# Performance work log

Measured on AMD Instinct MI355X. Metric: run time of the kernel, lower is better.

The kernel has to match this reference:

```python
import math
import jax, jax.numpy as jnp
import numpy as np

NUM_HEADS = 16
WINDOW = 64  # neighbor_size
NEG_INF = -1e30


def setup_inputs() -> dict:
    key = jax.random.key(0)
    ks = jax.random.split(key, 5)
    B, L, D = 2, 2048, 1024
    x = jax.random.normal(ks[0], (B, L, D), dtype=jnp.float32)
    s = 0.02
    Wq = jax.random.normal(ks[1], (D, D), dtype=jnp.float32) * s
    Wk = jax.random.normal(ks[2], (D, D), dtype=jnp.float32) * s
    Wv = jax.random.normal(ks[3], (D, D), dtype=jnp.float32) * s
    Wo = jax.random.normal(ks[4], (D, D), dtype=jnp.float32) * s
    return {
        "x": x, "Wq": Wq, "Wk": Wk, "Wv": Wv, "Wo": Wo,
        "sep_gate": jnp.float32(0.1),
        "align_gate": jnp.float32(0.1),
        "coh_gate": jnp.float32(0.1),
    }


def reference(x, Wq, Wk, Wv, Wo, sep_gate, align_gate, coh_gate):
    B, L, D = x.shape
    H = NUM_HEADS
    hd = D // H
    scale = math.sqrt(hd)

    # projections (torch Linear: y = x @ W.T), split heads -> (B, H, L, hd)
    def proj(W):
        return (x @ W.T).reshape(B, L, H, hd).transpose(0, 2, 1, 3)

    q, k, v = proj(Wq), proj(Wk), proj(Wv)

    # raw scores (B, H, L, L)
    scores = jnp.einsum("bhqd,bhkd->bhqk", q, k) / scale

    # Reynolds rules (applied BEFORE masking, mean over full kv dim, as in source)
    similarity = jax.nn.sigmoid(scores)
    separation = -sep_gate * similarity ** 2
    alignment = align_gate * scores
    score_mean = jnp.mean(scores, axis=-1, keepdims=True)
    cohesion = -coh_gate * jnp.abs(scores - score_mean)
    scores = scores + separation + alignment + cohesion

    # causal sliding-window mask: attend iff 0 <= i - j < WINDOW
    i = jnp.arange(L)[:, None]
    j = jnp.arange(L)[None, :]
    dist = i - j
    masked = (dist < 0) | (dist >= WINDOW)  # (L, L) True = blocked
    scores = jnp.where(masked[None, None, :, :], NEG_INF, scores)

    attn = jax.nn.softmax(scores, axis=-1)  # dropout p=0.0 -> identity
    out = jnp.einsum("bhqk,bhkd->bhqd", attn, v)
    out = out.transpose(0, 2, 1, 3).reshape(B, L, D)
    return out @ Wo.T
```

## Files before the change

kernel.cpp:

```cpp
#include <hip/hip_runtime.h>
#include <math.h>

#define L_SEQ 2048
#define DMODEL 1024
#define HEADS 16
#define HD 64
#define BATCH 2
#define MROWS (BATCH*L_SEQ)
#define KDIM 1024
#define VSTRIDE 2136

typedef short bfrag8 __attribute__((ext_vector_type(8)));
typedef float f32x4f __attribute__((ext_vector_type(4)));

__device__ __forceinline__ unsigned short f2bf(float f) {
    unsigned u = __float_as_uint(f);
    unsigned r = u + 0x7FFFu + ((u >> 16) & 1u);
    return (unsigned short)(r >> 16);
}
__device__ __forceinline__ float bf2f(unsigned short h) {
    return __uint_as_float(((unsigned)h) << 16);
}

__global__ __launch_bounds__(256) void convert_bf16(
    const float* __restrict__ x, const float* __restrict__ wq,
    const float* __restrict__ wk, const float* __restrict__ wv,
    const float* __restrict__ wo,
    unsigned short* __restrict__ xb, unsigned short* __restrict__ qwb,
    unsigned short* __restrict__ kwb, unsigned short* __restrict__ vwb,
    unsigned short* __restrict__ owb, float* __restrict__ kmean_acc)
{
    const int bid = blockIdx.x;
    if (bid == 8192) {
        float4 z = make_float4(0.f, 0.f, 0.f, 0.f);
        *(float4*)&kmean_acc[threadIdx.x * 8]     = z;
        *(float4*)&kmean_acc[threadIdx.x * 8 + 4] = z;
        return;
    }
    const float* src; unsigned short* dst; size_t base;
    if (bid < 4096) { src = x; dst = xb; base = (size_t)bid * 1024; }
    else {
        const int r = bid - 4096; const int w = r >> 10; const int off = r & 1023;
        src = (w==0) ? wq : (w==1) ? wk : (w==2) ? wv : wo;
        dst = (w==0) ? qwb : (w==1) ? kwb : (w==2) ? vwb : owb;
        base = (size_t)off * 1024;
    }
    const size_t idx = base + (size_t)threadIdx.x * 4;
    float4 v = *(const float4*)&src[idx];
    ushort4 o;
    o.x = f2bf(v.x); o.y = f2bf(v.y); o.z = f2bf(v.z); o.w = f2bf(v.w);
    *(ushort4*)&dst[idx] = o;
}

#define GBK 64

__global__ void mfma_gemm_qkv(
    const unsigned short* __restrict__ A,
    const unsigned short* __restrict__ W0, const unsigned short* __restrict__ W1,
    const unsigned short* __restrict__ W2,
    unsigned short* __restrict__ qo, unsigned short* __restrict__ ko,
    unsigned short* __restrict__ vo, float* __restrict__ kmean_acc)
{
    __shared__ short As[128*GBK];
    __shared__ short Bs[128*GBK];

    const int tid  = threadIdx.x;
    const int wave = tid >> 6, lane = tid & 63;
    const int m0   = blockIdx.x * 128;
    const int n0g  = blockIdx.y * 128;

    const int which = n0g >> 10;
    const int n0 = n0g & 1023;
    const unsigned short* Wp = (which==0) ? W0 : (which==1) ? W1 : W2;

    const int quad = lane >> 4, lm = lane & 15;
    const int wm = wave >> 1, wn = wave & 1;

    f32x4f acc[4][4] = {};

    const int se   = wave * 2048 + lane * 8;
    const int srow = se >> 6;
    const int scg  = (se & 63) >> 3;
    const int sgcol = ((scg ^ (srow & 7)) << 3);

    for (int k0 = 0; k0 < KDIM; k0 += GBK) {
        __syncthreads();
        #pragma unroll
        for (int i = 0; i < 4; ++i) {
            const int ebase = wave * 2048 + i * 512;
            const int row = srow + i * 8;
            __builtin_amdgcn_global_load_lds(
                (const __attribute__((address_space(1))) void*)(A + (size_t)(m0 + row) * KDIM + k0 + sgcol),
                (__attribute__((address_space(3))) void*)(&As[ebase]), 16, 0, 0);
            __builtin_amdgcn_global_load_lds(
                (const __attribute__((address_space(1))) void*)(Wp + (size_t)(n0 + row) * KDIM + k0 + sgcol),
                (__attribute__((address_space(3))) void*)(&Bs[ebase]), 16, 0, 0);
        }
        __syncthreads();

        #pragma unroll
        for (int kk = 0; kk < 2; ++kk) {
            bfrag8 af[4], bf[4];
            #pragma unroll
            for (int t = 0; t < 4; ++t) {
                const int ar = wm*64 + t*16 + lm;
                af[t] = *(const bfrag8*)&As[ar*GBK + (((kk*4 + quad) ^ (ar & 7)) << 3)];
                const int br = wn*64 + t*16 + lm;
                bf[t] = *(const bfrag8*)&Bs[br*GBK + (((kk*4 + quad) ^ (br & 7)) << 3)];
            }
            #pragma unroll
            for (int mt = 0; mt < 4; ++mt)
                #pragma unroll
                for (int nt = 0; nt < 4; ++nt)
                    acc[mt][nt] = __builtin_amdgcn_mfma_f32_16x16x32_bf16(
                        af[mt], bf[nt], acc[mt][nt], 0, 0, 0);
        }
    }

    if (which == 2) {
        #pragma unroll
        for (int mt = 0; mt < 4; ++mt)
            #pragma unroll
            for (int nt = 0; nt < 4; ++nt) {
                const int gn = n0 + wn*64 + nt*16 + lm;
                const int h = gn >> 6, d = gn & 63;
                const int gm0 = m0 + wm*64 + mt*16 + quad*4;
                const int b = gm0 >> 11, l0 = gm0 & (L_SEQ-1);
                ushort4 o;
                o.x = f2bf(acc[mt][nt][0]); o.y = f2bf(acc[mt][nt][1]);
                o.z = f2bf(acc[mt][nt][2]); o.w = f2bf(acc[mt][nt][3]);
                *(ushort4*)&vo[((size_t)((b*HEADS + h)*HD + d))*VSTRIDE + 64 + l0] = o;
            }
    } else {
        unsigned short* Cp = (which==0) ? qo : ko;
        #pragma unroll
        for (int mt = 0; mt < 4; ++mt)
            #pragma unroll
            for (int nt = 0; nt < 4; ++nt) {
                const int gn = n0 + wn*64 + nt*16 + lm;
                const int h = gn >> 6, d = gn & 63;
                #pragma unroll
                for (int r = 0; r < 4; ++r) {
                    const int gm = m0 + wm*64 + mt*16 + quad*4 + r;
                    const int b = gm >> 11, l = gm & (L_SEQ-1);
                    Cp[(((size_t)(b*HEADS + h) * L_SEQ) + l) * HD + d] = f2bf(acc[mt][nt][r]);
                }
            }
        if (which == 1) {
            const int b = m0 >> 11;
            #pragma unroll
            for (int nt = 0; nt < 4; ++nt) {
                const int gn = n0 + wn*64 + nt*16 + lm;
                const int h = gn >> 6, d = gn & 63;
                float s = 0.f;
                #pragma unroll
                for (int mt = 0; mt < 4; ++mt)
                    #pragma unroll
                    for (int r = 0; r < 4; ++r) s += acc[mt][nt][r];
                atomicAdd(&kmean_acc[(size_t)(b*HEADS + h)*HD + d], s);
            }
        }
    }
}

__global__ void out_proj_gemm(
    const unsigned short* __restrict__ A, const unsigned short* __restrict__ W,
    float* __restrict__ C)
{
    __shared__ short As[64*GBK];
    __shared__ short Bs[128*GBK];

    const int tid  = threadIdx.x;
    const int wave = tid >> 6, lane = tid & 63;
    const int m0   = blockIdx.x * 64;
    const int n0   = blockIdx.y * 128;

    const int quad = lane >> 4, lm = lane & 15;
    const int wm = wave >> 1, wn = wave & 1;

    f32x4f acc[2][4] = {};

    const int sea   = wave * 1024 + lane * 8;
    const int srowa = sea >> 6;
    const int sga   = ((((sea & 63) >> 3) ^ (srowa & 7)) << 3);
    const int seb   = wave * 2048 + lane * 8;
    const int srowb = seb >> 6;
    const int sgb   = ((((seb & 63) >> 3) ^ (srowb & 7)) << 3);

    for (int k0 = 0; k0 < KDIM; k0 += GBK) {
        __syncthreads();
        #pragma unroll
        for (int i = 0; i < 2; ++i) {
            const int ebase = wave * 1024 + i * 512;
            const int row = srowa + i * 8;
            __builtin_amdgcn_global_load_lds(
                (const __attribute__((address_space(1))) void*)(A + (size_t)(m0 + row) * KDIM + k0 + sga),
                (__attribute__((address_space(3))) void*)(&As[ebase]), 16, 0, 0);
        }
        #pragma unroll
        for (int i = 0; i < 4; ++i) {
            const int ebase = wave * 2048 + i * 512;
            const int row = srowb + i * 8;
            __builtin_amdgcn_global_load_lds(
                (const __attribute__((address_space(1))) void*)(W + (size_t)(n0 + row) * KDIM + k0 + sgb),
                (__attribute__((address_space(3))) void*)(&Bs[ebase]), 16, 0, 0);
        }
        __syncthreads();

        #pragma unroll
        for (int kk = 0; kk < 2; ++kk) {
            bfrag8 af[2], bf[4];
            #pragma unroll
            for (int t = 0; t < 2; ++t) {
                const int ar = wm*32 + t*16 + lm;
                af[t] = *(const bfrag8*)&As[ar*GBK + (((kk*4 + quad) ^ (ar & 7)) << 3)];
            }
            #pragma unroll
            for (int t = 0; t < 4; ++t) {
                const int br = wn*64 + t*16 + lm;
                bf[t] = *(const bfrag8*)&Bs[br*GBK + (((kk*4 + quad) ^ (br & 7)) << 3)];
            }
            #pragma unroll
            for (int mt = 0; mt < 2; ++mt)
                #pragma unroll
                for (int nt = 0; nt < 4; ++nt)
                    acc[mt][nt] = __builtin_amdgcn_mfma_f32_16x16x32_bf16(
                        af[mt], bf[nt], acc[mt][nt], 0, 0, 0);
        }
    }

    #pragma unroll
    for (int mt = 0; mt < 2; ++mt)
        #pragma unroll
        for (int nt = 0; nt < 4; ++nt) {
            const int gn = n0 + wn*64 + nt*16 + lm;
            #pragma unroll
            for (int r = 0; r < 4; ++r) {
                const int gm = m0 + wm*32 + mt*16 + quad*4 + r;
                C[(size_t)gm * DMODEL + gn] = acc[mt][nt][r];
            }
        }
}

#define P_STRIDE 104

__global__ __launch_bounds__(256) void attn_kernel(
    const unsigned short* __restrict__ qb, const unsigned short* __restrict__ kb,
    const unsigned short* __restrict__ vt, const float* __restrict__ kmean_acc,
    const float* __restrict__ g_sep, const float* __restrict__ g_align,
    const float* __restrict__ g_coh, unsigned short* __restrict__ out)
{
    __shared__ unsigned short pl[64 * P_STRIDE];

    const int tid = threadIdx.x;
    const int bh = blockIdx.x >> 5;
    const int qt = blockIdx.x & 31;
    const int q0 = qt * 64;
    const int j0 = q0 - 64;

    const int w = tid >> 6, lane = tid & 63;
    const int quad = lane >> 4, lm = lane & 15;
    const float sep = g_sep[0], align = g_align[0], coh = g_coh[0];

    const unsigned short* kbh = kb + (size_t)bh * L_SEQ * HD;
    const unsigned short* vbh = vt + (size_t)bh * HD * VSTRIDE;

    const unsigned short* qrow =
        qb + ((size_t)bh * L_SEQ + q0 + w*16 + lm) * HD + quad * 8;
    bfrag8 qa0 = *(const bfrag8*)qrow;
    bfrag8 qa1 = *(const bfrag8*)(qrow + 32);

    const float* kmp = kmean_acc + bh * HD + quad * 8;
    float4 km0 = *(const float4*)(kmp);
    float4 km1 = *(const float4*)(kmp + 4);
    float4 km2 = *(const float4*)(kmp + 32);
    float4 km3 = *(const float4*)(kmp + 36);
    float part =
        bf2f((unsigned short)qa0[0])*km0.x + bf2f((unsigned short)qa0[1])*km0.y +
        bf2f((unsigned short)qa0[2])*km0.z + bf2f((unsigned short)qa0[3])*km0.w +
        bf2f((unsigned short)qa0[4])*km1.x + bf2f((unsigned short)qa0[5])*km1.y +
        bf2f((unsigned short)qa0[6])*km1.z + bf2f((unsigned short)qa0[7])*km1.w +
        bf2f((unsigned short)qa1[0])*km2.x + bf2f((unsigned short)qa1[1])*km2.y +
        bf2f((unsigned short)qa1[2])*km2.z + bf2f((unsigned short)qa1[3])*km2.w +
        bf2f((unsigned short)qa1[4])*km3.x + bf2f((unsigned short)qa1[5])*km3.y +
        bf2f((unsigned short)qa1[6])*km3.z + bf2f((unsigned short)qa1[7])*km3.w;
    part *= (1.f / (float)L_SEQ);
    part += __shfl_xor(part, 16, 64);
    part += __shfl_xor(part, 32, 64);

    f32x4f sacc[6];
    #pragma unroll
    for (int t = 0; t < 6; ++t) {
        int kr = j0 + w*16 + t*16 + lm;
        kr = kr < 0 ? 0 : (kr >= L_SEQ ? L_SEQ - 1 : kr);
        const unsigned short* kp = kbh + (size_t)kr * HD + quad * 8;
        bfrag8 b0 = *(const bfrag8*)kp;
        bfrag8 b1 = *(const bfrag8*)(kp + 32);
        f32x4f z = {0.f, 0.f, 0.f, 0.f};
        z = __builtin_amdgcn_mfma_f32_16x16x32_bf16(qa0, b0, z, 0, 0, 0);
        sacc[t] = __builtin_amdgcn_mfma_f32_16x16x32_bf16(qa1, b1, z, 0, 0, 0);
    }

    float rinv[4];
    #pragma unroll
    for (int r = 0; r < 4; ++r) {
        const int row = quad*4 + r;
        const int i   = q0 + w*16 + row;
        const float mean_i = __shfl(part, row, 64) * 0.125f;
        float sc[6]; float mx = -3.0e38f;
        #pragma unroll
        for (int t = 0; t < 6; ++t) {
            const int jabs = j0 + w*16 + t*16 + lm;
            const int dist = i - jabs;
            float s = sacc[t][r] * 0.125f;
            const float sig = 1.f / (1.f + __expf(-s));
            float adj = s * (1.f + align) - sep * sig * sig - coh * fabsf(s - mean_i);
            const bool ok = (dist >= 0) && (dist < 64) && (jabs >= 0);
            sc[t] = ok ? adj : -3.0e38f;
            mx = fmaxf(mx, sc[t]);
        }
        mx = fmaxf(mx, __shfl_xor(mx, 1, 64));
        mx = fmaxf(mx, __shfl_xor(mx, 2, 64));
        mx = fmaxf(mx, __shfl_xor(mx, 4, 64));
        mx = fmaxf(mx, __shfl_xor(mx, 8, 64));
        float ls = 0.f;
        #pragma unroll
        for (int t = 0; t < 6; ++t) {
            const float p = __expf(sc[t] - mx);
            ls += p;
            pl[(w*16 + row) * P_STRIDE + t*16 + lm] = f2bf(p);
        }
        ls += __shfl_xor(ls, 1, 64);
        ls += __shfl_xor(ls, 2, 64);
        ls += __shfl_xor(ls, 4, 64);
        ls += __shfl_xor(ls, 8, 64);
        rinv[r] = 1.f / ls;
    }

    f32x4f oacc[4] = {};
    #pragma unroll
    for (int kk = 0; kk < 3; ++kk) {
        bfrag8 pa = *(const bfrag8*)&pl[(w*16 + lm) * P_STRIDE + kk*32 + quad*8];
        const int loff = 64 + j0 + w*16 + kk*32 + quad*8;
        #pragma unroll
        for (int nt = 0; nt < 4; ++nt) {
            bfrag8 bv = *(const bfrag8*)&vbh[(size_t)(nt*16 + lm) * VSTRIDE + loff];
            oacc[nt] = __builtin_amdgcn_mfma_f32_16x16x32_bf16(pa, bv, oacc[nt], 0, 0, 0);
        }
    }

    const int b = bh >> 4, h = bh & (HEADS - 1);
    #pragma unroll
    for (int nt = 0; nt < 4; ++nt)
        #pragma unroll
        for (int r = 0; r < 4; ++r) {
            const int i = q0 + w*16 + quad*4 + r;
            const int d = nt*16 + lm;
            out[((size_t)(b * L_SEQ + i)) * DMODEL + h * HD + d] =
                f2bf(oacc[nt][r] * rinv[r]);
        }
}

extern "C" void kernel_launch(void* const* d_in, const int* in_sizes, int n_in,
                              void* d_out, int out_size, void* d_ws, size_t ws_size,
                              hipStream_t stream)
{
    (void)in_sizes; (void)n_in; (void)out_size; (void)ws_size;
    const float* x     = (const float*)d_in[0];
    const float* Wq    = (const float*)d_in[1];
    const float* Wk    = (const float*)d_in[2];
    const float* Wv    = (const float*)d_in[3];
    const float* Wo    = (const float*)d_in[4];
    const float* g_sep   = (const float*)d_in[5];
    const float* g_align = (const float*)d_in[6];
    const float* g_coh   = (const float*)d_in[7];
    float* out = (float*)d_out;

    float* kmean_ws = (float*)d_ws;
    unsigned short* xb  = (unsigned short*)(kmean_ws + 2048);
    const size_t per = (size_t)MROWS * DMODEL;
    unsigned short* wqb = xb  + per;
    unsigned short* wkb = wqb + (size_t)DMODEL*KDIM;
    unsigned short* wvb = wkb + (size_t)DMODEL*KDIM;
    unsigned short* wob = wvb + (size_t)DMODEL*KDIM;
    unsigned short* qb  = wob + (size_t)DMODEL*KDIM;
    unsigned short* kb  = qb  + per;
    unsigned short* vtb = kb  + per;
    unsigned short* attb = vtb + (size_t)BATCH*HEADS*HD*VSTRIDE;

    convert_bf16<<<dim3(8193), dim3(256), 0, stream>>>(
        x, Wq, Wk, Wv, Wo, xb, wqb, wkb, wvb, wob, kmean_ws);
    mfma_gemm_qkv<<<dim3(MROWS/128, 3*DMODEL/128), dim3(256), 0, stream>>>(
        xb, wqb, wkb, wvb, qb, kb, vtb, kmean_ws);
    attn_kernel<<<dim3(BATCH*HEADS*(L_SEQ/64)), dim3(256), 0, stream>>>(
        qb, kb, vtb, kmean_ws, g_sep, g_align, g_coh, attb);
    out_proj_gemm<<<dim3(MROWS/64, DMODEL/128), dim3(256), 0, stream>>>(
        attb, wob, out);
}
```

Measured before the change: 160.3 us.

## Rewrite QKV GEMM as 256x256 tile with double-buffered staggered LDS pipeline

The QKV projection GEMM now uses 256x256 tiles computed by 512 threads (8 waves). LDS is double-buffered, and half-tile async global-to-LDS loads are interleaved between four MFMA quadrant phases using explicit waitcnt and barriers, with s_setprio raised around MFMA bursts. The goal is to hide memory latency behind matrix math and raise arithmetic intensity per block, in the style of the ping-pong schedules used in hipBLASLt. The cost is many more barriers, 128KB of LDS per block and fewer blocks (192), which may hurt occupancy or load balance.

```diff
diff --git a/kernel.cpp b/kernel.cpp
--- a/kernel.cpp
+++ b/kernel.cpp
@@ -53,110 +53,193 @@
 }
 
 #define GBK 64
-
-__global__ void mfma_gemm_qkv(
+#define NT16 (KDIM/64)
+
+__device__ __forceinline__ void stage_half(short* lds, int buf, int h,
+    const unsigned short* __restrict__ src, int rowbase, int ktile,
+    int srw, int sgc, int wb)
+{
+    const unsigned short* s0 =
+        src + (size_t)(rowbase + h*128 + srw) * KDIM + ktile*64 + sgc;
+    __builtin_amdgcn_global_load_lds(
+        (const __attribute__((address_space(1))) void*)s0,
+        (__attribute__((address_space(3))) void*)&lds[buf*16384 + h*8192 + wb],
+        16, 0, 0);
+    __builtin_amdgcn_global_load_lds(
+        (const __attribute__((address_space(1))) void*)(s0 + (size_t)64*KDIM),
+        (__attribute__((address_space(3))) void*)&lds[buf*16384 + h*8192 + 4096 + wb],
+        16, 0, 0);
+}
+
+__device__ __forceinline__ void read_a(const short* As, int base, int row0,
+                                       int lm, int quad, bfrag8 (&afh)[4][2])
+{
+#pragma unroll
+    for (int mt = 0; mt < 4; ++mt) {
+        const int ar = row0 + mt*16 + lm;
+        const int arb = base + ar*64;
+        afh[mt][0] = *(const bfrag8*)&As[arb + ((quad ^ (ar & 7)) << 3)];
+        afh[mt][1] = *(const bfrag8*)&As[arb + (((4 + quad) ^ (ar & 7)) << 3)];
+    }
+}
+
+__device__ __forceinline__ void read_b(const short* Bs, int base, int row0,
+                                       int lm, int quad, bfrag8 (&bf)[2][2])
+{
+#pragma unroll
+    for (int nt = 0; nt < 2; ++nt) {
+        const int br = row0 + nt*16 + lm;
+        const int brb = base + br*64;
+        bf[nt][0] = *(const bfrag8*)&Bs[brb + ((quad ^ (br & 7)) << 3)];
+        bf[nt][1] = *(const bfrag8*)&Bs[brb + (((4 + quad) ^ (br & 7)) << 3)];
+    }
+}
+
+__device__ __forceinline__ void mfma16(const bfrag8 (&afh)[4][2],
+                                       const bfrag8 (&bf)[2][2],
+                                       f32x4f (&acc)[8][4], int mh, int nh)
+{
+    __builtin_amdgcn_s_setprio(1);
+#pragma unroll
+    for (int mt = 0; mt < 4; ++mt)
+#pragma unroll
+        for (int nt = 0; nt < 2; ++nt) {
+            f32x4f a = acc[mh*4 + mt][nh*2 + nt];
+            a = __builtin_amdgcn_mfma_f32_16x16x32_bf16(afh[mt][0], bf[nt][0], a, 0, 0, 0);
+            a = __builtin_amdgcn_mfma_f32_16x16x32_bf16(afh[mt][1], bf[nt][1], a, 0, 0, 0);
+            acc[mh*4 + mt][nh*2 + nt] = a;
+        }
+    __builtin_amdgcn_s_setprio(0);
+}
+
+__global__ __launch_bounds__(512, 2) void mfma_gemm_qkv(
     const unsigned short* __restrict__ A,
     const unsigned short* __restrict__ W0, const unsigned short* __restrict__ W1,
     const unsigned short* __restrict__ W2,
     unsigned short* __restrict__ qo, unsigned short* __restrict__ ko,
     unsigned short* __restrict__ vo, float* __restrict__ kmean_acc)
 {
-    __shared__ short As[128*GBK];
-    __shared__ short Bs[128*GBK];
+    __shared__ short As[2*256*GBK];
+    __shared__ short Bs[2*256*GBK];
 
     const int tid  = threadIdx.x;
     const int wave = tid >> 6, lane = tid & 63;
-    const int m0   = blockIdx.x * 128;
-    const int n0g  = blockIdx.y * 128;
-
+    const int quad = lane >> 4, lm = lane & 15;
+    const int wm = wave >> 2, wn = wave & 3;
+
+    const int m0  = blockIdx.x * 256;
+    const int n0g = blockIdx.y * 256;
     const int which = n0g >> 10;
     const int n0 = n0g & 1023;
     const unsigned short* Wp = (which==0) ? W0 : (which==1) ? W1 : W2;
 
-    const int quad = lane >> 4, lm = lane & 15;
-    const int wm = wave >> 1, wn = wave & 1;
-
-    f32x4f acc[4][4] = {};
-
-    const int se   = wave * 2048 + lane * 8;
-    const int srow = se >> 6;
-    const int scg  = (se & 63) >> 3;
-    const int sgcol = ((scg ^ (srow & 7)) << 3);
-
-    for (int k0 = 0; k0 < KDIM; k0 += GBK) {
-        __syncthreads();
-        #pragma unroll
-        for (int i = 0; i < 4; ++i) {
-            const int ebase = wave * 2048 + i * 512;
-            const int row = srow + i * 8;
-            __builtin_amdgcn_global_load_lds(
-                (const __attribute__((address_space(1))) void*)(A + (size_t)(m0 + row) * KDIM + k0 + sgcol),
-                (__attribute__((address_space(3))) void*)(&As[ebase]), 16, 0, 0);
-            __builtin_amdgcn_global_load_lds(
-                (const __attribute__((address_space(1))) void*)(Wp + (size_t)(n0 + row) * KDIM + k0 + sgcol),
-                (__attribute__((address_space(3))) void*)(&Bs[ebase]), 16, 0, 0);
-        }
-        __syncthreads();
-
-        #pragma unroll
-        for (int kk = 0; kk < 2; ++kk) {
-            bfrag8 af[4], bf[4];
-            #pragma unroll
-            for (int t = 0; t < 4; ++t) {
-                const int ar = wm*64 + t*16 + lm;
-                af[t] = *(const bfrag8*)&As[ar*GBK + (((kk*4 + quad) ^ (ar & 7)) << 3)];
-                const int br = wn*64 + t*16 + lm;
-                bf[t] = *(const bfrag8*)&Bs[br*GBK + (((kk*4 + quad) ^ (br & 7)) << 3)];
-            }
-            #pragma unroll
-            for (int mt = 0; mt < 4; ++mt)
-                #pragma unroll
-                for (int nt = 0; nt < 4; ++nt)
-                    acc[mt][nt] = __builtin_amdgcn_mfma_f32_16x16x32_bf16(
-                        af[mt], bf[nt], acc[mt][nt], 0, 0, 0);
-        }
+    const int srw = tid >> 3;
+    const int sgc = (((tid & 7) ^ (srw & 7)) << 3);
+    const int wb  = wave << 9;
+
+    stage_half(As, 0, 0, A,  m0, 0, srw, sgc, wb);
+    stage_half(Bs, 0, 0, Wp, n0, 0, srw, sgc, wb);
+    stage_half(Bs, 0, 1, Wp, n0, 0, srw, sgc, wb);
+    stage_half(As, 0, 1, A,  m0, 0, srw, sgc, wb);
+    asm volatile("s_waitcnt vmcnt(4)" ::: "memory");
+    stage_half(As, 1, 0, A,  m0, 1, srw, sgc, wb);
+    stage_half(Bs, 1, 0, Wp, n0, 1, srw, sgc, wb);
+    stage_half(Bs, 1, 1, Wp, n0, 1, srw, sgc, wb);
+    asm volatile("s_waitcnt vmcnt(6)" ::: "memory");
+    __builtin_amdgcn_s_barrier();
+
+    bfrag8 afh[4][2], bf0[2][2], bf1[2][2];
+    f32x4f acc[8][4] = {};
+
+    for (int t = 0; t < NT16; ++t) {
+        const int cur = t & 1, nxt = cur ^ 1;
+        const int cb = cur * 16384;
+
+        read_a(As, cb, wm*64, lm, quad, afh);
+        read_b(Bs, cb, wn*32, lm, quad, bf0);
+        if (t + 1 < NT16) stage_half(As, nxt, 1, A, m0, t+1, srw, sgc, wb);
+        asm volatile("s_waitcnt lgkmcnt(8)" ::: "memory");
+        __builtin_amdgcn_s_barrier();
+        asm volatile("s_waitcnt lgkmcnt(0)" ::: "memory");
+        mfma16(afh, bf0, acc, 0, 0);
+        __builtin_amdgcn_s_barrier();
+
+        read_b(Bs, cb, 128 + wn*32, lm, quad, bf1);
+        if (t + 2 < NT16) stage_half(As, cur, 0, A, m0, t+2, srw, sgc, wb);
+        __builtin_amdgcn_s_barrier();
+        asm volatile("s_waitcnt lgkmcnt(0)" ::: "memory");
+        mfma16(afh, bf1, acc, 0, 1);
+        __builtin_amdgcn_s_barrier();
+
+        read_a(As, cb, 128 + wm*64, lm, quad, afh);
+        if (t + 2 < NT16) stage_half(Bs, cur, 0, Wp, n0, t+2, srw, sgc, wb);
+        __builtin_amdgcn_s_barrier();
+        asm volatile("s_waitcnt lgkmcnt(0)" ::: "memory");
+        mfma16(afh, bf1, acc, 1, 1);
+        __builtin_amdgcn_s_barrier();
+
+        if (t + 2 < NT16) stage_half(Bs, cur, 1, Wp, n0, t+2, srw, sgc, wb);
+        __builtin_amdgcn_s_barrier();
+        mfma16(afh, bf0, acc, 1, 0);
+        if (t < NT16 - 2)       { asm volatile("s_waitcnt vmcnt(6)" ::: "memory"); }
+        else if (t == NT16 - 2) { asm volatile("s_waitcnt vmcnt(0)" ::: "memory"); }
+        __builtin_amdgcn_s_barrier();
     }
 
     if (which == 2) {
-        #pragma unroll
+#pragma unroll
+        for (int mh = 0; mh < 2; ++mh)
+#pragma unroll
         for (int mt = 0; mt < 4; ++mt)
-            #pragma unroll
-            for (int nt = 0; nt < 4; ++nt) {
-                const int gn = n0 + wn*64 + nt*16 + lm;
-                const int h = gn >> 6, d = gn & 63;
-                const int gm0 = m0 + wm*64 + mt*16 + quad*4;
-                const int b = gm0 >> 11, l0 = gm0 & (L_SEQ-1);
-                ushort4 o;
-                o.x = f2bf(acc[mt][nt][0]); o.y = f2bf(acc[mt][nt][1]);
-                o.z = f2bf(acc[mt][nt][2]); o.w = f2bf(acc[mt][nt][3]);
-                *(ushort4*)&vo[((size_t)((b*HEADS + h)*HD + d))*VSTRIDE + 64 + l0] = o;
-            }
+#pragma unroll
+        for (int nh = 0; nh < 2; ++nh)
+#pragma unroll
+        for (int nt = 0; nt < 2; ++nt) {
+            const int gn = n0 + nh*128 + wn*32 + nt*16 + lm;
+            const int h = gn >> 6, d = gn & 63;
+            const int gm0 = m0 + mh*128 + wm*64 + mt*16 + quad*4;
+            const int b = gm0 >> 11, l0 = gm0 & (L_SEQ-1);
+            const f32x4f a = acc[mh*4+mt][nh*2+nt];
+            ushort4 o;
+            o.x = f2bf(a[0]); o.y = f2bf(a[1]);
+            o.z = f2bf(a[2]); o.w = f2bf(a[3]);
+            *(ushort4*)&vo[((size_t)((b*HEADS + h)*HD + d))*VSTRIDE + 64 + l0] = o;
+        }
     } else {
         unsigned short* Cp = (which==0) ? qo : ko;
-        #pragma unroll
+#pragma unroll
+        for (int mh = 0; mh < 2; ++mh)
+#pragma unroll
         for (int mt = 0; mt < 4; ++mt)
-            #pragma unroll
-            for (int nt = 0; nt < 4; ++nt) {
-                const int gn = n0 + wn*64 + nt*16 + lm;
-                const int h = gn >> 6, d = gn & 63;
-                #pragma unroll
-                for (int r = 0; r < 4; ++r) {
-                    const int gm = m0 + wm*64 + mt*16 + quad*4 + r;
-                    const int b = gm >> 11, l = gm & (L_SEQ-1);
-                    Cp[(((size_t)(b*HEADS + h) * L_SEQ) + l) * HD + d] = f2bf(acc[mt][nt][r]);
-                }
+#pragma unroll
+        for (int nh = 0; nh < 2; ++nh)
+#pragma unroll
+        for (int nt = 0; nt < 2; ++nt) {
+            const int gn = n0 + nh*128 + wn*32 + nt*16 + lm;
+            const int h = gn >> 6, d = gn & 63;
+            const f32x4f a = acc[mh*4+mt][nh*2+nt];
+#pragma unroll
+            for (int r = 0; r < 4; ++r) {
+                const int gm = m0 + mh*128 + wm*64 + mt*16 + quad*4 + r;
+                const int b = gm >> 11, l = gm & (L_SEQ-1);
+                Cp[(((size_t)(b*HEADS + h) * L_SEQ) + l) * HD + d] = f2bf(a[r]);
             }
+        }
         if (which == 1) {
             const int b = m0 >> 11;
-            #pragma unroll
-            for (int nt = 0; nt < 4; ++nt) {
-                const int gn = n0 + wn*64 + nt*16 + lm;
+#pragma unroll
+            for (int nh = 0; nh < 2; ++nh)
+#pragma unroll
+            for (int nt = 0; nt < 2; ++nt) {
+                const int gn = n0 + nh*128 + wn*32 + nt*16 + lm;
                 const int h = gn >> 6, d = gn & 63;
                 float s = 0.f;
-                #pragma unroll
+#pragma unroll
+                for (int mh = 0; mh < 2; ++mh)
+#pragma unroll
                 for (int mt = 0; mt < 4; ++mt)
-                    #pragma unroll
-                    for (int r = 0; r < 4; ++r) s += acc[mt][nt][r];
+#pragma unroll
+                for (int r = 0; r < 4; ++r) s += acc[mh*4+mt][nh*2+nt][r];
                 atomicAdd(&kmean_acc[(size_t)(b*HEADS + h)*HD + d], s);
             }
         }
@@ -390,7 +473,7 @@
 
     convert_bf16<<<dim3(8193), dim3(256), 0, stream>>>(
         x, Wq, Wk, Wv, Wo, xb, wqb, wkb, wvb, wob, kmean_ws);
-    mfma_gemm_qkv<<<dim3(MROWS/128, 3*DMODEL/128), dim3(256), 0, stream>>>(
+    mfma_gemm_qkv<<<dim3(MROWS/256, 3*DMODEL/256), dim3(512), 0, stream>>>(
         xb, wqb, wkb, wvb, qb, kb, vtb, kmean_ws);
     attn_kernel<<<dim3(BATCH*HEADS*(L_SEQ/64)), dim3(256), 0, stream>>>(
         qb, kb, vtb, kmean_ws, g_sep, g_align, g_coh, attb);
```

Measured after the change: 163.1 us. No clear change (+1.7%).

## Restructure QKV GEMM into double-buffered 256x192 tiles with staged async loads

Applied to the files above, without the earlier changes.

Rewrites the fused QKV projection GEMM to use 512-thread blocks computing 256x192 output tiles over a single concatenated weight matrix. LDS is double-buffered and global-to-LDS loads for upcoming k-tiles are spread across three compute phases, synchronised with explicit waitcnt and barriers and with raised wave priority during MFMA bursts. The block index is swizzled for cache locality. The aim is to hide memory latency behind MFMA work and cut per-tile load overhead. In exchange the kernel uses more LDS and registers, and it relies on Wq/Wk/Wv being stored contiguously.

```diff
diff --git a/kernel.cpp b/kernel.cpp
--- a/kernel.cpp
+++ b/kernel.cpp
@@ -53,111 +53,197 @@
 }
 
 #define GBK 64
-
-__global__ void mfma_gemm_qkv(
+#define NT16 (KDIM/64)
+
+__device__ __forceinline__ void sround(short* ldsreg, const unsigned short* greg,
+                                       int ktile, int srw, int sgc, int wb)
+{
+    __builtin_amdgcn_global_load_lds(
+        (const __attribute__((address_space(1))) void*)(greg + (size_t)srw * KDIM + (ktile << 6) + sgc),
+        (__attribute__((address_space(3))) void*)(ldsreg + wb), 16, 0, 0);
+}
+
+__global__ __launch_bounds__(512, 2) void mfma_gemm_qkv(
     const unsigned short* __restrict__ A,
-    const unsigned short* __restrict__ W0, const unsigned short* __restrict__ W1,
-    const unsigned short* __restrict__ W2,
+    const unsigned short* __restrict__ W,
     unsigned short* __restrict__ qo, unsigned short* __restrict__ ko,
     unsigned short* __restrict__ vo, float* __restrict__ kmean_acc)
 {
-    __shared__ short As[128*GBK];
-    __shared__ short Bs[128*GBK];
+    __shared__ short As[2*256*GBK];
+    __shared__ short Bs[2*192*GBK];
 
     const int tid  = threadIdx.x;
     const int wave = tid >> 6, lane = tid & 63;
-    const int m0   = blockIdx.x * 128;
-    const int n0g  = blockIdx.y * 128;
-
-    const int which = n0g >> 10;
-    const int n0 = n0g & 1023;
-    const unsigned short* Wp = (which==0) ? W0 : (which==1) ? W1 : W2;
-
     const int quad = lane >> 4, lm = lane & 15;
     const int wm = wave >> 1, wn = wave & 1;
 
-    f32x4f acc[4][4] = {};
-
-    const int se   = wave * 2048 + lane * 8;
-    const int srow = se >> 6;
-    const int scg  = (se & 63) >> 3;
-    const int sgcol = ((scg ^ (srow & 7)) << 3);
-
-    for (int k0 = 0; k0 < KDIM; k0 += GBK) {
-        __syncthreads();
-        #pragma unroll
-        for (int i = 0; i < 4; ++i) {
-            const int ebase = wave * 2048 + i * 512;
-            const int row = srow + i * 8;
-            __builtin_amdgcn_global_load_lds(
-                (const __attribute__((address_space(1))) void*)(A + (size_t)(m0 + row) * KDIM + k0 + sgcol),
-                (__attribute__((address_space(3))) void*)(&As[ebase]), 16, 0, 0);
-            __builtin_amdgcn_global_load_lds(
-                (const __attribute__((address_space(1))) void*)(Wp + (size_t)(n0 + row) * KDIM + k0 + sgcol),
-                (__attribute__((address_space(3))) void*)(&Bs[ebase]), 16, 0, 0);
-        }
-        __syncthreads();
-
-        #pragma unroll
-        for (int kk = 0; kk < 2; ++kk) {
-            bfrag8 af[4], bf[4];
-            #pragma unroll
-            for (int t = 0; t < 4; ++t) {
-                const int ar = wm*64 + t*16 + lm;
-                af[t] = *(const bfrag8*)&As[ar*GBK + (((kk*4 + quad) ^ (ar & 7)) << 3)];
-                const int br = wn*64 + t*16 + lm;
-                bf[t] = *(const bfrag8*)&Bs[br*GBK + (((kk*4 + quad) ^ (br & 7)) << 3)];
-            }
-            #pragma unroll
-            for (int mt = 0; mt < 4; ++mt)
-                #pragma unroll
-                for (int nt = 0; nt < 4; ++nt)
-                    acc[mt][nt] = __builtin_amdgcn_mfma_f32_16x16x32_bf16(
-                        af[mt], bf[nt], acc[mt][nt], 0, 0, 0);
-        }
-    }
-
-    if (which == 2) {
-        #pragma unroll
+    const int raw = blockIdx.x + (blockIdx.y << 4);
+    const int swz = ((raw & 7) << 5) + (raw >> 3);
+    const int m0  = (swz & 15) * 256;
+    const int n0g = (swz >> 4) * 192;
+
+    const int srw = tid >> 3;
+    const int sgc = (((tid & 7) ^ (srw & 7)) << 3);
+    const int wb  = wave << 9;
+
+    const unsigned short* Ar0 = A + (size_t)m0 * KDIM;
+    const unsigned short* Ar1 = Ar0 + (size_t)64  * KDIM;
+    const unsigned short* Ar2 = Ar0 + (size_t)128 * KDIM;
+    const unsigned short* Ar3 = Ar0 + (size_t)192 * KDIM;
+    const unsigned short* Br0 = W + (size_t)n0g * KDIM;
+    const unsigned short* Br1 = Br0 + (size_t)64  * KDIM;
+    const unsigned short* Br2 = Br0 + (size_t)128 * KDIM;
+
+    sround(As,          Ar0, 0, srw, sgc, wb);
+    sround(As +  4096,  Ar1, 0, srw, sgc, wb);
+    sround(Bs,          Br0, 0, srw, sgc, wb);
+    sround(As +  8192,  Ar2, 0, srw, sgc, wb);
+    sround(As + 12288,  Ar3, 0, srw, sgc, wb);
+    sround(Bs +  4096,  Br1, 0, srw, sgc, wb);
+    sround(Bs +  8192,  Br2, 0, srw, sgc, wb);
+    sround(As + 16384,  Ar0, 1, srw, sgc, wb);
+    sround(As + 20480,  Ar1, 1, srw, sgc, wb);
+    sround(Bs + 12288,  Br0, 1, srw, sgc, wb);
+    sround(As + 24576,  Ar2, 1, srw, sgc, wb);
+    sround(As + 28672,  Ar3, 1, srw, sgc, wb);
+    sround(Bs + 16384,  Br1, 1, srw, sgc, wb);
+    asm volatile("s_waitcnt vmcnt(6)" ::: "memory");
+    __builtin_amdgcn_s_barrier();
+
+    bfrag8 af[4][2], bfp[2][2];
+    f32x4f acc[4][6] = {};
+
+    for (int t = 0; t < NT16; ++t) {
+        const int cur = t & 1, nxt = cur ^ 1;
+        const int ca = cur * 16384;
+        const int cb = cur * 12288;
+
+#pragma unroll
+        for (int mt = 0; mt < 4; ++mt) {
+            const int ar = wm*64 + mt*16 + lm;
+            const int ab = ca + ar*64;
+            af[mt][0] = *(const bfrag8*)&As[ab + ((quad ^ (ar & 7)) << 3)];
+            af[mt][1] = *(const bfrag8*)&As[ab + (((4 + quad) ^ (ar & 7)) << 3)];
+        }
+#pragma unroll
+        for (int j = 0; j < 2; ++j) {
+            const int br = (2*(0*2 + j) + wn)*16 + lm;
+            const int bb = cb + br*64;
+            bfp[j][0] = *(const bfrag8*)&Bs[bb + ((quad ^ (br & 7)) << 3)];
+            bfp[j][1] = *(const bfrag8*)&Bs[bb + (((4 + quad) ^ (br & 7)) << 3)];
+        }
+        if (t + 1 < NT16) sround(Bs + nxt*12288 + 8192, Br2, t+1, srw, sgc, wb);
+        asm volatile("s_waitcnt lgkmcnt(8)" ::: "memory");
+        __builtin_amdgcn_s_barrier();
+        asm volatile("s_waitcnt lgkmcnt(0)" ::: "memory");
+        __builtin_amdgcn_s_setprio(1);
+#pragma unroll
         for (int mt = 0; mt < 4; ++mt)
-            #pragma unroll
-            for (int nt = 0; nt < 4; ++nt) {
-                const int gn = n0 + wn*64 + nt*16 + lm;
-                const int h = gn >> 6, d = gn & 63;
+#pragma unroll
+            for (int j = 0; j < 2; ++j) {
+                f32x4f a = acc[mt][j];
+                a = __builtin_amdgcn_mfma_f32_16x16x32_bf16(af[mt][0], bfp[j][0], a, 0, 0, 0);
+                a = __builtin_amdgcn_mfma_f32_16x16x32_bf16(af[mt][1], bfp[j][1], a, 0, 0, 0);
+                acc[mt][j] = a;
+            }
+        __builtin_amdgcn_s_setprio(0);
+        __builtin_amdgcn_s_barrier();
+
+#pragma unroll
+        for (int j = 0; j < 2; ++j) {
+            const int br = (2*(1*2 + j) + wn)*16 + lm;
+            const int bb = cb + br*64;
+            bfp[j][0] = *(const bfrag8*)&Bs[bb + ((quad ^ (br & 7)) << 3)];
+            bfp[j][1] = *(const bfrag8*)&Bs[bb + (((4 + quad) ^ (br & 7)) << 3)];
+        }
+        if (t + 2 < NT16) {
+            sround(As + ca,        Ar0, t+2, srw, sgc, wb);
+            sround(As + ca + 4096, Ar1, t+2, srw, sgc, wb);
+            sround(Bs + cb,        Br0, t+2, srw, sgc, wb);
+        }
+        __builtin_amdgcn_s_barrier();
+        asm volatile("s_waitcnt lgkmcnt(0)" ::: "memory");
+        __builtin_amdgcn_s_setprio(1);
+#pragma unroll
+        for (int mt = 0; mt < 4; ++mt)
+#pragma unroll
+            for (int j = 0; j < 2; ++j) {
+                f32x4f a = acc[mt][2 + j];
+                a = __builtin_amdgcn_mfma_f32_16x16x32_bf16(af[mt][0], bfp[j][0], a, 0, 0, 0);
+                a = __builtin_amdgcn_mfma_f32_16x16x32_bf16(af[mt][1], bfp[j][1], a, 0, 0, 0);
+                acc[mt][2 + j] = a;
+            }
+        __builtin_amdgcn_s_setprio(0);
+        __builtin_amdgcn_s_barrier();
+
+#pragma unroll
+        for (int j = 0; j < 2; ++j) {
+            const int br = (2*(2*2 + j) + wn)*16 + lm;
+            const int bb = cb + br*64;
+            bfp[j][0] = *(const bfrag8*)&Bs[bb + ((quad ^ (br & 7)) << 3)];
+            bfp[j][1] = *(const bfrag8*)&Bs[bb + (((4 + quad) ^ (br & 7)) << 3)];
+        }
+        if (t + 2 < NT16) {
+            sround(As + ca +  8192, Ar2, t+2, srw, sgc, wb);
+            sround(As + ca + 12288, Ar3, t+2, srw, sgc, wb);
+            sround(Bs + cb +  4096, Br1, t+2, srw, sgc, wb);
+        }
+        __builtin_amdgcn_s_barrier();
+        asm volatile("s_waitcnt lgkmcnt(0)" ::: "memory");
+        __builtin_amdgcn_s_setprio(1);
+#pragma unroll
+        for (int mt = 0; mt < 4; ++mt)
+#pragma unroll
+            for (int j = 0; j < 2; ++j) {
+                f32x4f a = acc[mt][4 + j];
+                a = __builtin_amdgcn_mfma_f32_16x16x32_bf16(af[mt][0], bfp[j][0], a, 0, 0, 0);
+                a = __builtin_amdgcn_mfma_f32_16x16x32_bf16(af[mt][1], bfp[j][1], a, 0, 0, 0);
+                acc[mt][4 + j] = a;
+            }
+        __builtin_amdgcn_s_setprio(0);
+        if (t < NT16 - 2)       { asm volatile("s_waitcnt vmcnt(6)" ::: "memory"); }
+        else if (t == NT16 - 2) { asm volatile("s_waitcnt vmcnt(0)" ::: "memory"); }
+        __builtin_amdgcn_s_barrier();
+    }
+
+    const int bq = m0 >> 11;
+#pragma unroll
+    for (int nt = 0; nt < 6; ++nt) {
+        const int fn  = 2*nt + wn;
+        const int gng = n0g + fn*16 + lm;
+        const int which = gng >> 10;
+        const int gn = gng & 1023;
+        const int h = gn >> 6, d = gn & 63;
+        if (which == 2) {
+#pragma unroll
+            for (int mt = 0; mt < 4; ++mt) {
                 const int gm0 = m0 + wm*64 + mt*16 + quad*4;
-                const int b = gm0 >> 11, l0 = gm0 & (L_SEQ-1);
+                const int l0  = gm0 & (L_SEQ-1);
+                const f32x4f a = acc[mt][nt];
                 ushort4 o;
-                o.x = f2bf(acc[mt][nt][0]); o.y = f2bf(acc[mt][nt][1]);
-                o.z = f2bf(acc[mt][nt][2]); o.w = f2bf(acc[mt][nt][3]);
-                *(ushort4*)&vo[((size_t)((b*HEADS + h)*HD + d))*VSTRIDE + 64 + l0] = o;
-            }
-    } else {
-        unsigned short* Cp = (which==0) ? qo : ko;
-        #pragma unroll
-        for (int mt = 0; mt < 4; ++mt)
-            #pragma unroll
-            for (int nt = 0; nt < 4; ++nt) {
-                const int gn = n0 + wn*64 + nt*16 + lm;
-                const int h = gn >> 6, d = gn & 63;
-                #pragma unroll
+                o.x = f2bf(a[0]); o.y = f2bf(a[1]);
+                o.z = f2bf(a[2]); o.w = f2bf(a[3]);
+                *(ushort4*)&vo[((size_t)((bq*HEADS + h)*HD + d))*VSTRIDE + 64 + l0] = o;
+            }
+        } else {
+            unsigned short* Cp = (which==0) ? qo : ko;
+#pragma unroll
+            for (int mt = 0; mt < 4; ++mt) {
+                const f32x4f a = acc[mt][nt];
+#pragma unroll
                 for (int r = 0; r < 4; ++r) {
                     const int gm = m0 + wm*64 + mt*16 + quad*4 + r;
-                    const int b = gm >> 11, l = gm & (L_SEQ-1);
-                    Cp[(((size_t)(b*HEADS + h) * L_SEQ) + l) * HD + d] = f2bf(acc[mt][nt][r]);
+                    const int l = gm & (L_SEQ-1);
+                    Cp[(((size_t)(bq*HEADS + h) * L_SEQ) + l) * HD + d] = f2bf(a[r]);
                 }
             }
-        if (which == 1) {
-            const int b = m0 >> 11;
-            #pragma unroll
-            for (int nt = 0; nt < 4; ++nt) {
-                const int gn = n0 + wn*64 + nt*16 + lm;
-                const int h = gn >> 6, d = gn & 63;
+            if (which == 1) {
                 float s = 0.f;
-                #pragma unroll
+#pragma unroll
                 for (int mt = 0; mt < 4; ++mt)
-                    #pragma unroll
+#pragma unroll
                     for (int r = 0; r < 4; ++r) s += acc[mt][nt][r];
-                atomicAdd(&kmean_acc[(size_t)(b*HEADS + h)*HD + d], s);
+                atomicAdd(&kmean_acc[(size_t)(bq*HEADS + h)*HD + d], s);
             }
         }
     }
@@ -390,8 +476,8 @@
 
     convert_bf16<<<dim3(8193), dim3(256), 0, stream>>>(
         x, Wq, Wk, Wv, Wo, xb, wqb, wkb, wvb, wob, kmean_ws);
-    mfma_gemm_qkv<<<dim3(MROWS/128, 3*DMODEL/128), dim3(256), 0, stream>>>(
-        xb, wqb, wkb, wvb, qb, kb, vtb, kmean_ws);
+    mfma_gemm_qkv<<<dim3(16, 16), dim3(512), 0, stream>>>(
+        xb, wqb, qb, kb, vtb, kmean_ws);
     attn_kernel<<<dim3(BATCH*HEADS*(L_SEQ/64)), dim3(256), 0, stream>>>(
         qb, kb, vtb, kmean_ws, g_sep, g_align, g_coh, attb);
     out_proj_gemm<<<dim3(MROWS/64, DMODEL/128), dim3(256), 0, stream>>>(
```

Result: slower. 172.4 us (+7.5%).
